# Kernel tuning notes

Measured on AMD Instinct MI355X. Metric: run time of the kernel, lower is better.

## Reference

```python
import jax, jax.numpy as jnp
import numpy as np

DIM = 1024
NUM_HEADS = 16
HEAD_DIM = DIM // NUM_HEADS
SCALE = HEAD_DIM ** -0.5


def setup_inputs() -> dict:
    key = jax.random.key(0)
    ks = jax.random.split(key, 6)
    B, N, C = 2, 2048, DIM
    std = 1.0 / np.sqrt(C)
    x = jax.random.normal(ks[0], (B, N, C), dtype=jnp.float32)
    wq = jax.random.normal(ks[1], (C, C), dtype=jnp.float32) * std
    wk = jax.random.normal(ks[2], (C, C), dtype=jnp.float32) * std
    wv = jax.random.normal(ks[3], (C, C), dtype=jnp.float32) * std
    w_proj = jax.random.normal(ks[4], (C, C), dtype=jnp.float32) * std
    b_proj = jax.random.normal(ks[5], (C,), dtype=jnp.float32) * 0.01
    return {"x": x, "wq": wq, "wk": wk, "wv": wv, "w_proj": w_proj, "b_proj": b_proj}


def reference(x, wq, wk, wv, w_proj, b_proj):
    B, N, C = x.shape
    H, D = NUM_HEADS, HEAD_DIM
    Nq = N // 2
    # q from first half of tokens; k, v from all tokens
    q = (x[:, :Nq] @ wq.T).reshape(B, Nq, H, D).transpose(0, 2, 1, 3)  # [B,H,Nq,D]
    k = (x @ wk.T).reshape(B, N, H, D).transpose(0, 2, 1, 3)           # [B,H,N,D]
    v = (x @ wv.T).reshape(B, N, H, D).transpose(0, 2, 1, 3)           # [B,H,N,D]
    attn = jnp.einsum('bhqd,bhkd->bhqk', q, k) * SCALE
    attn = jax.nn.softmax(attn, axis=-1)
    out = jnp.einsum('bhqk,bhkd->bhqd', attn, v)                       # [B,H,Nq,D]
    out = out.transpose(0, 2, 1, 3).reshape(B, Nq, C)
    return out @ w_proj.T + b_proj
```

## Files before the change

kernel.cpp:

```cpp
#include <hip/hip_runtime.h>

typedef _Float16 f16;
typedef _Float16 f16x8 __attribute__((ext_vector_type(8)));
typedef _Float16 f16x4 __attribute__((ext_vector_type(4)));
typedef float f32x4 __attribute__((ext_vector_type(4)));

#define MFMA_F16(a, b, c) __builtin_amdgcn_mfma_f32_16x16x32_f16(a, b, c, 0, 0, 0)

__device__ __forceinline__ void gld16(const void* g, void* l) {
  __builtin_amdgcn_global_load_lds(
      (const __attribute__((address_space(1))) unsigned int*)(unsigned long long)g,
      (__attribute__((address_space(3))) unsigned int*)(unsigned long long)l, 16, 0, 0);
}

__global__ __launch_bounds__(256) void cvt_x_kernel(const float* __restrict__ in,
                                                    f16* __restrict__ out, int n8) {
  int i = blockIdx.x * 256 + threadIdx.x;
  if (i >= n8) return;
  const float4* p = (const float4*)(in + (size_t)i * 8);
  float4 a = p[0], b = p[1];
  f16x8 o = {(f16)a.x, (f16)a.y, (f16)a.z, (f16)a.w,
             (f16)b.x, (f16)b.y, (f16)b.z, (f16)b.w};
  *(f16x8*)(out + (size_t)i * 8) = o;
}

__global__ __launch_bounds__(256) void cvt_w4_kernel(const float* __restrict__ w0,
                                                     const float* __restrict__ w1,
                                                     const float* __restrict__ w2,
                                                     const float* __restrict__ w3,
                                                     f16* __restrict__ out) {
  int i = blockIdx.x * 256 + threadIdx.x;
  int t = i >> 17, r = i & 131071;
  const float* w = (t == 0) ? w0 : (t == 1) ? w1 : (t == 2) ? w2 : w3;
  const float4* p = (const float4*)(w + (size_t)r * 8);
  float4 a = p[0], b = p[1];
  f16x8 o = {(f16)a.x, (f16)a.y, (f16)a.z, (f16)a.w,
             (f16)b.x, (f16)b.y, (f16)b.z, (f16)b.w};
  *(f16x8*)(out + (size_t)t * 1048576 + (size_t)r * 8) = o;
}

__global__ __launch_bounds__(256) void qkv_gemm_kernel(
    const f16* __restrict__ A, const f16* __restrict__ Wq,
    const f16* __restrict__ Wk, const f16* __restrict__ Wv,
    f16* __restrict__ Qo, f16* __restrict__ Ko, f16* __restrict__ VT) {
  __shared__ __align__(16) f16 As[2][128 * 64];
  __shared__ __align__(16) f16 Bs[2][128 * 64];
  const int bid = blockIdx.x + blockIdx.y * 8;
  const int swz = (bid & 7) * 80 + (bid >> 3);
  const int bx = swz & 7, y = swz >> 3;
  const f16* Bw;
  f16* Co = nullptr;
  int mt, isv = 0;
  if (y < 16) { Bw = Wq; Co = Qo; mt = (y & 7) | ((y >> 3) << 4); }
  else if (y < 48) { Bw = Wk; Co = Ko; mt = y - 16; }
  else { Bw = Wv; isv = 1; mt = y - 48; }
  const int m0 = mt * 128, n0 = bx * 128;
  const int tid = threadIdx.x, lane = tid & 63, w = tid >> 6;
  const int wr = w >> 1, wc = w & 1, g = lane >> 4, c = lane & 15;
  const int r_st = tid >> 3, t_st = tid & 7;

  auto stage = [&](int k0, int buf) {
#pragma unroll
    for (int i = 0; i < 4; ++i) {
      int row = r_st + i * 32;
      int sl = (t_st ^ (row & 7)) * 8;
      gld16(&A[(size_t)(m0 + row) * 1024 + k0 + sl], &As[buf][(row * 8 + t_st) * 8]);
      gld16(&Bw[(size_t)(n0 + row) * 1024 + k0 + sl], &Bs[buf][(row * 8 + t_st) * 8]);
    }
  };

  f32x4 acc[4][4] = {};

  stage(0, 0);
  __syncthreads();

  for (int t = 0; t < 16; ++t) {
    const int cur = t & 1;
    if (t < 15) stage((t + 1) * 64, cur ^ 1);
#pragma unroll
    for (int kb = 0; kb < 2; ++kb) {
      f16x8 af[4], bf[4];
#pragma unroll
      for (int m2 = 0; m2 < 4; ++m2)
        af[m2] = *(const f16x8*)&As[cur][(wr * 64 + m2 * 16 + c) * 64 +
                                         (((kb * 4 + g) ^ (c & 7)) * 8)];
#pragma unroll
      for (int nt = 0; nt < 4; ++nt)
        bf[nt] = *(const f16x8*)&Bs[cur][(wc * 64 + nt * 16 + c) * 64 +
                                         (((kb * 4 + g) ^ (c & 7)) * 8)];
#pragma unroll
      for (int m2 = 0; m2 < 4; ++m2)
#pragma unroll
        for (int nt = 0; nt < 4; ++nt)
          acc[m2][nt] = MFMA_F16(af[m2], bf[nt], acc[m2][nt]);
    }
    __syncthreads();
  }

  if (isv) {
    const int b = m0 >> 11;
    const int n_base = (m0 & 2047) + wr * 64 + g * 4;
#pragma unroll
    for (int m2 = 0; m2 < 4; ++m2)
#pragma unroll
      for (int nt = 0; nt < 4; ++nt) {
        int col = n0 + wc * 64 + nt * 16 + c;
        int h = col >> 6, d = col & 63;
        f16x4 pv = {(f16)acc[m2][nt][0], (f16)acc[m2][nt][1],
                    (f16)acc[m2][nt][2], (f16)acc[m2][nt][3]};
        *(f16x4*)&VT[((size_t)((b * 16 + h) * 64 + d)) * 2048 + n_base + m2 * 16] = pv;
      }
  } else {
#pragma unroll
    for (int m2 = 0; m2 < 4; ++m2)
#pragma unroll
      for (int nt = 0; nt < 4; ++nt) {
        int col = n0 + wc * 64 + nt * 16 + c;
#pragma unroll
        for (int r = 0; r < 4; ++r)
          Co[(size_t)(m0 + wr * 64 + m2 * 16 + g * 4 + r) * 1024 + col] =
              (f16)acc[m2][nt][r];
      }
  }
}

__global__ __launch_bounds__(256) void proj_gemm_kernel(
    const f16* __restrict__ A, const f16* __restrict__ Bw,
    float* __restrict__ C, const float* __restrict__ bias) {
  __shared__ __align__(16) f16 As[2][64 * 64];
  __shared__ __align__(16) f16 Bs[2][64 * 64];
  const int bid = blockIdx.x + blockIdx.y * 16;
  const int swz = (bid & 7) * 64 + (bid >> 3);
  const int m0 = (swz >> 4) * 64, n0 = (swz & 15) * 64;
  const int tid = threadIdx.x, lane = tid & 63, w = tid >> 6;
  const int wr = w >> 1, wc = w & 1, g = lane >> 4, c = lane & 15;
  const int r_st = tid >> 3, t_st = tid & 7;

  auto stage = [&](int k0, int buf) {
#pragma unroll
    for (int i = 0; i < 2; ++i) {
      int row = r_st + i * 32;
      int sl = (t_st ^ (row & 7)) * 8;
      gld16(&A[(size_t)(m0 + row) * 1024 + k0 + sl], &As[buf][(row * 8 + t_st) * 8]);
      gld16(&Bw[(size_t)(n0 + row) * 1024 + k0 + sl], &Bs[buf][(row * 8 + t_st) * 8]);
    }
  };

  f32x4 acc[2][2] = {};

  stage(0, 0);
  __syncthreads();

  for (int t = 0; t < 16; ++t) {
    const int cur = t & 1;
    if (t < 15) stage((t + 1) * 64, cur ^ 1);
#pragma unroll
    for (int kb = 0; kb < 2; ++kb) {
      f16x8 af[2], bf[2];
#pragma unroll
      for (int m2 = 0; m2 < 2; ++m2)
        af[m2] = *(const f16x8*)&As[cur][(wr * 32 + m2 * 16 + c) * 64 +
                                         (((kb * 4 + g) ^ (c & 7)) * 8)];
#pragma unroll
      for (int nt = 0; nt < 2; ++nt)
        bf[nt] = *(const f16x8*)&Bs[cur][(wc * 32 + nt * 16 + c) * 64 +
                                         (((kb * 4 + g) ^ (c & 7)) * 8)];
#pragma unroll
      for (int m2 = 0; m2 < 2; ++m2)
#pragma unroll
        for (int nt = 0; nt < 2; ++nt)
          acc[m2][nt] = MFMA_F16(af[m2], bf[nt], acc[m2][nt]);
    }
    __syncthreads();
  }

#pragma unroll
  for (int m2 = 0; m2 < 2; ++m2)
#pragma unroll
    for (int nt = 0; nt < 2; ++nt) {
      int col = n0 + wc * 32 + nt * 16 + c;
      float bv = bias[col];
#pragma unroll
      for (int r = 0; r < 4; ++r)
        C[(size_t)(m0 + wr * 32 + m2 * 16 + g * 4 + r) * 1024 + col] =
            acc[m2][nt][r] + bv;
    }
}

__global__ __launch_bounds__(256, 4) void attn_kernel(const f16* __restrict__ Q,
                                                      const f16* __restrict__ Kg,
                                                      const f16* __restrict__ VT,
                                                      f16* __restrict__ Opart,
                                                      float2* __restrict__ ML) {
  __shared__ __align__(16) f16 Ks[2][64 * 64];
  __shared__ __align__(16) f16 Vs[2][64 * 64];
  __shared__ __align__(16) f16 Ps[4][16 * 64];
  const int flat = blockIdx.x + blockIdx.y * 16 + blockIdx.z * 256;
  const int swz = (flat & 7) * 128 + (flat >> 3);
  const int qt = swz & 15, h = (swz >> 4) & 15;
  const int b = (swz >> 9) & 1, ch = (swz >> 8) & 1;
  const int tid = threadIdx.x, lane = tid & 63, w = tid >> 6;
  const int g = lane >> 4, c = lane & 15;
  const int r_st = tid >> 3, t_st = tid & 7;

  const f16* Kbase = Kg + (size_t)(b * 2048 + ch * 1024) * 1024 + h * 64;
  const f16* Vbase = VT + ((size_t)((b * 16 + h) * 64)) * 2048 + ch * 1024;

  f16x8 qf[2];
  {
    const f16* qp = Q + (size_t)(b * 2048 + qt * 64 + w * 16 + c) * 1024 + h * 64;
    qf[0] = *(const f16x8*)(qp + g * 8);
    qf[1] = *(const f16x8*)(qp + 32 + g * 8);
#pragma unroll
    for (int j = 0; j < 8; ++j) {
      qf[0][j] = (f16)((float)qf[0][j] * 0.1803368801f);
      qf[1][j] = (f16)((float)qf[1][j] * 0.1803368801f);
    }
  }

  auto stage = [&](int t, int buf) {
#pragma unroll
    for (int i = 0; i < 2; ++i) {
      int row = r_st + i * 32;
      int sl = (t_st ^ (row & 7)) * 8;
      gld16(&Kbase[(size_t)(t * 64 + row) * 1024 + sl],
            &Ks[buf][(row * 8 + t_st) * 8]);
      gld16(&Vbase[(size_t)row * 2048 + t * 64 + sl],
            &Vs[buf][(row * 8 + t_st) * 8]);
    }
  };

  f32x4 oacc[4] = {};
  float l_run = 0.f;

  stage(0, 0);
  __syncthreads();

  for (int t = 0; t < 16; ++t) {
    const int cur = t & 1;
    if (t < 15) stage(t + 1, cur ^ 1);

    f32x4 s[4] = {};
#pragma unroll
    for (int kt = 0; kt < 4; ++kt) {
      f16x8 kf0 = *(const f16x8*)&Ks[cur][(kt * 16 + c) * 64 + ((g ^ (c & 7)) * 8)];
      f16x8 kf1 =
          *(const f16x8*)&Ks[cur][(kt * 16 + c) * 64 + (((4 + g) ^ (c & 7)) * 8)];
      s[kt] = MFMA_F16(kf0, qf[0], s[kt]);
      s[kt] = MFMA_F16(kf1, qf[1], s[kt]);
    }

    float rsum = 0.f;
#pragma unroll
    for (int kt = 0; kt < 4; ++kt)
#pragma unroll
      for (int r = 0; r < 4; ++r) {
        float p = exp2f(s[kt][r]);
        s[kt][r] = p;
        rsum += p;
      }
    rsum += __shfl_xor(rsum, 16);
    rsum += __shfl_xor(rsum, 32);
    l_run += rsum;

#pragma unroll
    for (int kt = 0; kt < 4; ++kt) {
      f16x4 pv = {(f16)s[kt][0], (f16)s[kt][1], (f16)s[kt][2], (f16)s[kt][3]};
      *(f16x4*)&Ps[w][c * 64 + (((kt * 2 + (g >> 1)) ^ (c & 7)) * 8) + (g & 1) * 4] =
          pv;
    }

#pragma unroll
    for (int kb = 0; kb < 2; ++kb) {
      f16x8 pf = *(const f16x8*)&Ps[w][c * 64 + (((kb * 4 + g) ^ (c & 7)) * 8)];
#pragma unroll
      for (int dt = 0; dt < 4; ++dt) {
        f16x8 vf = *(const f16x8*)&Vs[cur][(dt * 16 + c) * 64 +
                                           (((kb * 4 + g) ^ (c & 7)) * 8)];
        oacc[dt] = MFMA_F16(pf, vf, oacc[dt]);
      }
    }

    __syncthreads();
  }

  float li[4];
#pragma unroll
  for (int r = 0; r < 4; ++r) li[r] = 1.f / __shfl(l_run, g * 4 + r);
#pragma unroll
  for (int dt = 0; dt < 4; ++dt)
#pragma unroll
    for (int r = 0; r < 4; ++r) {
      Opart[(size_t)ch * 2097152 +
            (size_t)(b * 1024 + qt * 64 + w * 16 + g * 4 + r) * 1024 + h * 64 +
            dt * 16 + c] = (f16)(oacc[dt][r] * li[r]);
    }
  if (lane < 16)
    ML[ch * 32768 + (b * 1024 + qt * 64 + w * 16 + lane) * 16 + h] =
        make_float2(0.f, l_run);
}

__global__ __launch_bounds__(256) void combine_kernel(const f16* __restrict__ Opart,
                                                      const float2* __restrict__ ML,
                                                      f16* __restrict__ O16) {
  int i = blockIdx.x * 256 + threadIdx.x;
  int row = i >> 7;
  int h = (i & 127) >> 3;
  float2 a = ML[row * 16 + h];
  float2 bml = ML[32768 + row * 16 + h];
  float m = fmaxf(a.x, bml.x);
  float w0 = exp2f(a.x - m) * a.y;
  float w1 = exp2f(bml.x - m) * bml.y;
  float inv = 1.f / (w0 + w1);
  float a0 = w0 * inv, a1 = w1 * inv;
  f16x8 o0 = *(const f16x8*)&Opart[(size_t)i * 8];
  f16x8 o1 = *(const f16x8*)&Opart[2097152 + (size_t)i * 8];
  f16x8 r;
#pragma unroll
  for (int j = 0; j < 8; ++j) r[j] = (f16)(a0 * (float)o0[j] + a1 * (float)o1[j]);
  *(f16x8*)&O16[(size_t)i * 8] = r;
}

extern "C" void kernel_launch(void* const* d_in, const int* in_sizes, int n_in,
                              void* d_out, int out_size, void* d_ws, size_t ws_size,
                              hipStream_t stream) {
  const float* x = (const float*)d_in[0];
  const float* wq = (const float*)d_in[1];
  const float* wk = (const float*)d_in[2];
  const float* wv = (const float*)d_in[3];
  const float* wp = (const float*)d_in[4];
  const float* bp = (const float*)d_in[5];
  float* out = (float*)d_out;

  char* p = (char*)d_ws;
  f16* x16 = (f16*)p;  p += (size_t)4194304 * 2;
  f16* w16 = (f16*)p;  p += (size_t)4 * 1048576 * 2;
  f16* Q16 = (f16*)p;  p += (size_t)4194304 * 2;
  f16* K16 = (f16*)p;  p += (size_t)4194304 * 2;
  f16* Opart = (f16*)p; p += (size_t)4194304 * 2;
  f16* VT16 = (f16*)p; p += (size_t)4194304 * 2;
  f16* O16 = (f16*)p;  p += (size_t)2097152 * 2;

  f16* wq16 = w16;
  f16* wk16 = w16 + 1048576;
  f16* wv16 = w16 + 2 * 1048576;
  f16* wp16 = w16 + 3 * 1048576;

  cvt_x_kernel<<<4194304 / 8 / 256, 256, 0, stream>>>(x, x16, 4194304 / 8);
  cvt_w4_kernel<<<4 * 131072 / 256, 256, 0, stream>>>(wq, wk, wv, wp, w16);

  qkv_gemm_kernel<<<dim3(8, 80), 256, 0, stream>>>(x16, wq16, wk16, wv16, Q16, K16,
                                                   VT16);

  float2* MLp = (float2*)x16;
  attn_kernel<<<dim3(16, 16, 4), 256, 0, stream>>>(Q16, K16, VT16, Opart, MLp);
  combine_kernel<<<1024, 256, 0, stream>>>(Opart, MLp, O16);

  proj_gemm_kernel<<<dim3(16, 32), 256, 0, stream>>>(O16, wp16, out, bp);
}
```

Baseline: 96.30 us.

## Split attention keys into four chunks with 128-query tiles and single-buffered V

The attention kernel now processes 128 queries per block (32 per wave) and splits the key range into four chunks of 512 instead of two of 1024. Each K/V tile is therefore reused across twice as many queries. V is single-buffered and loaded after the PV step, with explicit vmcnt waits and barriers. The PV product is computed transposed so the output can be written as vectors. The combine kernel now merges four partial outputs, which doubles the Opart workspace and its traffic, and occupancy is lowered to 3 blocks per CU.

```diff
diff --git a/kernel.cpp b/kernel.cpp
--- a/kernel.cpp
+++ b/kernel.cpp
@@ -187,137 +187,177 @@
     }
 }
 
-__global__ __launch_bounds__(256, 4) void attn_kernel(const f16* __restrict__ Q,
+__global__ __launch_bounds__(256, 3) void attn_kernel(const f16* __restrict__ Q,
                                                       const f16* __restrict__ Kg,
                                                       const f16* __restrict__ VT,
                                                       f16* __restrict__ Opart,
-                                                      float2* __restrict__ ML) {
+                                                      float* __restrict__ ML) {
   __shared__ __align__(16) f16 Ks[2][64 * 64];
-  __shared__ __align__(16) f16 Vs[2][64 * 64];
-  __shared__ __align__(16) f16 Ps[4][16 * 64];
-  const int flat = blockIdx.x + blockIdx.y * 16 + blockIdx.z * 256;
+  __shared__ __align__(16) f16 Vs[64 * 64];
+  __shared__ __align__(16) f16 Ps[4][32 * 64];
+  const int flat = blockIdx.x;
   const int swz = (flat & 7) * 128 + (flat >> 3);
-  const int qt = swz & 15, h = (swz >> 4) & 15;
-  const int b = (swz >> 9) & 1, ch = (swz >> 8) & 1;
+  const int qt = swz & 7, h = (swz >> 3) & 15;
+  const int ch = (swz >> 7) & 3, b = swz >> 9;
   const int tid = threadIdx.x, lane = tid & 63, w = tid >> 6;
   const int g = lane >> 4, c = lane & 15;
   const int r_st = tid >> 3, t_st = tid & 7;
 
-  const f16* Kbase = Kg + (size_t)(b * 2048 + ch * 1024) * 1024 + h * 64;
-  const f16* Vbase = VT + ((size_t)((b * 16 + h) * 64)) * 2048 + ch * 1024;
-
-  f16x8 qf[2];
-  {
-    const f16* qp = Q + (size_t)(b * 2048 + qt * 64 + w * 16 + c) * 1024 + h * 64;
-    qf[0] = *(const f16x8*)(qp + g * 8);
-    qf[1] = *(const f16x8*)(qp + 32 + g * 8);
+  const f16* Kbase = Kg + (size_t)(b * 2048 + ch * 512) * 1024 + h * 64;
+  const f16* Vbase = VT + ((size_t)((b * 16 + h) * 64)) * 2048 + ch * 512;
+
+  f16x8 qf[2][2];
+#pragma unroll
+  for (int qs = 0; qs < 2; ++qs) {
+    const f16* qp =
+        Q + (size_t)(b * 2048 + qt * 128 + w * 32 + qs * 16 + c) * 1024 + h * 64;
+    qf[qs][0] = *(const f16x8*)(qp + g * 8);
+    qf[qs][1] = *(const f16x8*)(qp + 32 + g * 8);
 #pragma unroll
     for (int j = 0; j < 8; ++j) {
-      qf[0][j] = (f16)((float)qf[0][j] * 0.1803368801f);
-      qf[1][j] = (f16)((float)qf[1][j] * 0.1803368801f);
-    }
-  }
-
-  auto stage = [&](int t, int buf) {
+      qf[qs][0][j] = (f16)((float)qf[qs][0][j] * 0.1803368801f);
+      qf[qs][1][j] = (f16)((float)qf[qs][1][j] * 0.1803368801f);
+    }
+  }
+
+  auto stageK = [&](int t, int buf) {
 #pragma unroll
     for (int i = 0; i < 2; ++i) {
       int row = r_st + i * 32;
       int sl = (t_st ^ (row & 7)) * 8;
       gld16(&Kbase[(size_t)(t * 64 + row) * 1024 + sl],
             &Ks[buf][(row * 8 + t_st) * 8]);
-      gld16(&Vbase[(size_t)row * 2048 + t * 64 + sl],
-            &Vs[buf][(row * 8 + t_st) * 8]);
     }
   };
-
-  f32x4 oacc[4] = {};
-  float l_run = 0.f;
-
-  stage(0, 0);
-  __syncthreads();
-
-  for (int t = 0; t < 16; ++t) {
+  auto stageV = [&](int t) {
+#pragma unroll
+    for (int i = 0; i < 2; ++i) {
+      int row = r_st + i * 32;
+      int sl = (t_st ^ (row & 7)) * 8;
+      gld16(&Vbase[(size_t)row * 2048 + t * 64 + sl], &Vs[(row * 8 + t_st) * 8]);
+    }
+  };
+
+  f32x4 oaccT[4][2] = {};
+  float l_part[2] = {0.f, 0.f};
+
+  stageK(0, 0);
+  stageV(0);
+  asm volatile("s_waitcnt vmcnt(0)" ::: "memory");
+  __builtin_amdgcn_s_barrier();
+  __builtin_amdgcn_sched_barrier(0);
+
+  for (int t = 0; t < 8; ++t) {
     const int cur = t & 1;
-    if (t < 15) stage(t + 1, cur ^ 1);
-
-    f32x4 s[4] = {};
-#pragma unroll
-    for (int kt = 0; kt < 4; ++kt) {
-      f16x8 kf0 = *(const f16x8*)&Ks[cur][(kt * 16 + c) * 64 + ((g ^ (c & 7)) * 8)];
-      f16x8 kf1 =
-          *(const f16x8*)&Ks[cur][(kt * 16 + c) * 64 + (((4 + g) ^ (c & 7)) * 8)];
-      s[kt] = MFMA_F16(kf0, qf[0], s[kt]);
-      s[kt] = MFMA_F16(kf1, qf[1], s[kt]);
-    }
-
-    float rsum = 0.f;
-#pragma unroll
-    for (int kt = 0; kt < 4; ++kt)
-#pragma unroll
-      for (int r = 0; r < 4; ++r) {
-        float p = exp2f(s[kt][r]);
-        s[kt][r] = p;
-        rsum += p;
+    if (t < 7) stageK(t + 1, cur ^ 1);
+
+#pragma unroll
+    for (int qs = 0; qs < 2; ++qs) {
+      f32x4 s[4] = {};
+#pragma unroll
+      for (int kt = 0; kt < 4; ++kt) {
+        f16x8 kf0 =
+            *(const f16x8*)&Ks[cur][(kt * 16 + c) * 64 + ((g ^ (c & 7)) * 8)];
+        f16x8 kf1 =
+            *(const f16x8*)&Ks[cur][(kt * 16 + c) * 64 + (((4 + g) ^ (c & 7)) * 8)];
+        s[kt] = MFMA_F16(kf0, qf[qs][0], s[kt]);
+        s[kt] = MFMA_F16(kf1, qf[qs][1], s[kt]);
       }
-    rsum += __shfl_xor(rsum, 16);
-    rsum += __shfl_xor(rsum, 32);
-    l_run += rsum;
-
-#pragma unroll
-    for (int kt = 0; kt < 4; ++kt) {
-      f16x4 pv = {(f16)s[kt][0], (f16)s[kt][1], (f16)s[kt][2], (f16)s[kt][3]};
-      *(f16x4*)&Ps[w][c * 64 + (((kt * 2 + (g >> 1)) ^ (c & 7)) * 8) + (g & 1) * 4] =
-          pv;
-    }
+      float rs = 0.f;
+#pragma unroll
+      for (int kt = 0; kt < 4; ++kt)
+#pragma unroll
+        for (int r = 0; r < 4; ++r) {
+          float p = exp2f(s[kt][r]);
+          s[kt][r] = p;
+          rs += p;
+        }
+      l_part[qs] += rs;
+#pragma unroll
+      for (int kt = 0; kt < 4; ++kt) {
+        f16x4 pv = {(f16)s[kt][0], (f16)s[kt][1], (f16)s[kt][2], (f16)s[kt][3]};
+        *(f16x4*)&Ps[w][(qs * 16 + c) * 64 +
+                        (((kt * 2 + (g >> 1)) ^ (c & 7)) * 8) + (g & 1) * 4] = pv;
+      }
+    }
+
+    if (t < 7) {
+      asm volatile("s_waitcnt vmcnt(2)" ::: "memory");
+    } else {
+      asm volatile("s_waitcnt vmcnt(0)" ::: "memory");
+    }
+    __builtin_amdgcn_s_barrier();
+    __builtin_amdgcn_sched_barrier(0);
 
 #pragma unroll
     for (int kb = 0; kb < 2; ++kb) {
-      f16x8 pf = *(const f16x8*)&Ps[w][c * 64 + (((kb * 4 + g) ^ (c & 7)) * 8)];
+      f16x8 pf0 =
+          *(const f16x8*)&Ps[w][c * 64 + (((kb * 4 + g) ^ (c & 7)) * 8)];
+      f16x8 pf1 =
+          *(const f16x8*)&Ps[w][(16 + c) * 64 + (((kb * 4 + g) ^ (c & 7)) * 8)];
 #pragma unroll
       for (int dt = 0; dt < 4; ++dt) {
-        f16x8 vf = *(const f16x8*)&Vs[cur][(dt * 16 + c) * 64 +
-                                           (((kb * 4 + g) ^ (c & 7)) * 8)];
-        oacc[dt] = MFMA_F16(pf, vf, oacc[dt]);
+        f16x8 vf = *(const f16x8*)&Vs[(dt * 16 + c) * 64 +
+                                      (((kb * 4 + g) ^ (c & 7)) * 8)];
+        oaccT[dt][0] = MFMA_F16(vf, pf0, oaccT[dt][0]);
+        oaccT[dt][1] = MFMA_F16(vf, pf1, oaccT[dt][1]);
       }
     }
 
-    __syncthreads();
-  }
-
-  float li[4];
-#pragma unroll
-  for (int r = 0; r < 4; ++r) li[r] = 1.f / __shfl(l_run, g * 4 + r);
-#pragma unroll
-  for (int dt = 0; dt < 4; ++dt)
-#pragma unroll
-    for (int r = 0; r < 4; ++r) {
-      Opart[(size_t)ch * 2097152 +
-            (size_t)(b * 1024 + qt * 64 + w * 16 + g * 4 + r) * 1024 + h * 64 +
-            dt * 16 + c] = (f16)(oacc[dt][r] * li[r]);
-    }
-  if (lane < 16)
-    ML[ch * 32768 + (b * 1024 + qt * 64 + w * 16 + lane) * 16 + h] =
-        make_float2(0.f, l_run);
+    asm volatile("s_waitcnt vmcnt(0)" ::: "memory");
+    __builtin_amdgcn_s_barrier();
+    __builtin_amdgcn_sched_barrier(0);
+    if (t < 7) stageV(t + 1);
+  }
+
+  float lf[2];
+#pragma unroll
+  for (int qs = 0; qs < 2; ++qs) {
+    float l = l_part[qs];
+    l += __shfl_xor(l, 16);
+    l += __shfl_xor(l, 32);
+    lf[qs] = l;
+  }
+#pragma unroll
+  for (int qs = 0; qs < 2; ++qs) {
+    float li = 1.f / lf[qs];
+#pragma unroll
+    for (int dt = 0; dt < 4; ++dt) {
+      f16x4 ov = {(f16)(oaccT[dt][qs][0] * li), (f16)(oaccT[dt][qs][1] * li),
+                  (f16)(oaccT[dt][qs][2] * li), (f16)(oaccT[dt][qs][3] * li)};
+      *(f16x4*)&Opart[(size_t)ch * 2097152 +
+                      (size_t)(b * 1024 + qt * 128 + w * 32 + qs * 16 + c) * 1024 +
+                      h * 64 + dt * 16 + g * 4] = ov;
+    }
+  }
+  if (lane < 16) {
+#pragma unroll
+    for (int qs = 0; qs < 2; ++qs)
+      ML[ch * 32768 + (b * 1024 + qt * 128 + w * 32 + qs * 16 + lane) * 16 + h] =
+          lf[qs];
+  }
 }
 
 __global__ __launch_bounds__(256) void combine_kernel(const f16* __restrict__ Opart,
-                                                      const float2* __restrict__ ML,
+                                                      const float* __restrict__ ML,
                                                       f16* __restrict__ O16) {
   int i = blockIdx.x * 256 + threadIdx.x;
   int row = i >> 7;
   int h = (i & 127) >> 3;
-  float2 a = ML[row * 16 + h];
-  float2 bml = ML[32768 + row * 16 + h];
-  float m = fmaxf(a.x, bml.x);
-  float w0 = exp2f(a.x - m) * a.y;
-  float w1 = exp2f(bml.x - m) * bml.y;
-  float inv = 1.f / (w0 + w1);
-  float a0 = w0 * inv, a1 = w1 * inv;
+  float l0 = ML[row * 16 + h];
+  float l1 = ML[32768 + row * 16 + h];
+  float l2 = ML[65536 + row * 16 + h];
+  float l3 = ML[98304 + row * 16 + h];
+  float inv = 1.f / (l0 + l1 + l2 + l3);
   f16x8 o0 = *(const f16x8*)&Opart[(size_t)i * 8];
   f16x8 o1 = *(const f16x8*)&Opart[2097152 + (size_t)i * 8];
+  f16x8 o2 = *(const f16x8*)&Opart[4194304 + (size_t)i * 8];
+  f16x8 o3 = *(const f16x8*)&Opart[6291456 + (size_t)i * 8];
   f16x8 r;
 #pragma unroll
-  for (int j = 0; j < 8; ++j) r[j] = (f16)(a0 * (float)o0[j] + a1 * (float)o1[j]);
+  for (int j = 0; j < 8; ++j)
+    r[j] = (f16)((l0 * (float)o0[j] + l1 * (float)o1[j] + l2 * (float)o2[j] +
+                  l3 * (float)o3[j]) * inv);
   *(f16x8*)&O16[(size_t)i * 8] = r;
 }
 
@@ -333,13 +373,13 @@
   float* out = (float*)d_out;
 
   char* p = (char*)d_ws;
-  f16* x16 = (f16*)p;  p += (size_t)4194304 * 2;
-  f16* w16 = (f16*)p;  p += (size_t)4 * 1048576 * 2;
-  f16* Q16 = (f16*)p;  p += (size_t)4194304 * 2;
-  f16* K16 = (f16*)p;  p += (size_t)4194304 * 2;
-  f16* Opart = (f16*)p; p += (size_t)4194304 * 2;
-  f16* VT16 = (f16*)p; p += (size_t)4194304 * 2;
-  f16* O16 = (f16*)p;  p += (size_t)2097152 * 2;
+  f16* x16 = (f16*)p;   p += (size_t)4194304 * 2;
+  f16* w16 = (f16*)p;   p += (size_t)4 * 1048576 * 2;
+  f16* Q16 = (f16*)p;   p += (size_t)4194304 * 2;
+  f16* K16 = (f16*)p;   p += (size_t)4194304 * 2;
+  f16* VT16 = (f16*)p;  p += (size_t)4194304 * 2;
+  f16* Opart = (f16*)p; p += (size_t)8388608 * 2;
+  f16* O16 = (f16*)p;   p += (size_t)2097152 * 2;
 
   f16* wq16 = w16;
   f16* wk16 = w16 + 1048576;
@@ -352,8 +392,8 @@
   qkv_gemm_kernel<<<dim3(8, 80), 256, 0, stream>>>(x16, wq16, wk16, wv16, Q16, K16,
                                                    VT16);
 
-  float2* MLp = (float2*)x16;
-  attn_kernel<<<dim3(16, 16, 4), 256, 0, stream>>>(Q16, K16, VT16, Opart, MLp);
+  float* MLp = (float*)x16;
+  attn_kernel<<<dim3(1024), 256, 0, stream>>>(Q16, K16, VT16, Opart, MLp);
   combine_kernel<<<1024, 256, 0, stream>>>(Opart, MLp, O16);
 
   proj_gemm_kernel<<<dim3(16, 32), 256, 0, stream>>>(O16, wp16, out, bp);
```

Result: no change. 95.89 us (-0.4%).
